# Performance work log

Hardware: AMD Instinct MI355X
Metric: run time of the kernel (lower is better)

Reference implementation:

```python
import jax, jax.numpy as jnp
import numpy as np

B, H, SQ, SK, D, INT, F = 1, 32, 2048, 2048, 128, 128, 32
THOLD = 0.5


def _mlp(x, W1, b1, W2, b2, W3, b3):
    # x: [b,h,s,d]; W*: [h,out,in] (torch Linear layout), y = x @ W^T + b, per head
    h = jax.nn.silu(jnp.einsum('bhsd,hid->bhsi', x, W1) + b1[None, :, None, :])
    h = jax.nn.silu(jnp.einsum('bhsi,hji->bhsj', h, W2) + b2[None, :, None, :])
    return jnp.einsum('bhsj,hfj->bhsf', h, W3) + b3[None, :, None, :]


def setup_inputs() -> dict:
    key = jax.random.key(0)
    ks = jax.random.split(key, 16)
    sc = 0.05  # small init so tanh stays in its linear-ish range
    inp = {
        'K': jax.random.normal(ks[0], (B, H, SK, D), jnp.float32),
        'Q': jax.random.normal(ks[1], (B, H, SQ, D), jnp.float32),
        'Wk1': jax.random.normal(ks[2], (H, INT, D), jnp.float32) * sc,
        'bk1': jax.random.normal(ks[3], (H, INT), jnp.float32) * sc,
        'Wk2': jax.random.normal(ks[4], (H, INT, INT), jnp.float32) * sc,
        'bk2': jax.random.normal(ks[5], (H, INT), jnp.float32) * sc,
        'Wk3': jax.random.normal(ks[6], (H, F, INT), jnp.float32) * sc,
        'bk3': jax.random.normal(ks[7], (H, F), jnp.float32) * sc,
        'Wq1': jax.random.normal(ks[8], (H, INT, D), jnp.float32) * sc,
        'bq1': jax.random.normal(ks[9], (H, INT), jnp.float32) * sc,
        'Wq2': jax.random.normal(ks[10], (H, INT, INT), jnp.float32) * sc,
        'bq2': jax.random.normal(ks[11], (H, INT), jnp.float32) * sc,
        'Wq3': jax.random.normal(ks[12], (H, F, INT), jnp.float32) * sc,
        'bq3': jax.random.normal(ks[13], (H, F), jnp.float32) * sc,
    }
    return inp


def reference(K, Q, Wk1, bk1, Wk2, bk2, Wk3, bk3, Wq1, bq1, Wq2, bq2, Wq3, bq3):
    # soft (hard=False) path of USA.forward
    Kl = jnp.tanh(_mlp(K, Wk1, bk1, Wk2, bk2, Wk3, bk3))  # [b,h,sk,F]
    Ql = jnp.tanh(_mlp(Q, Wq1, bq1, Wq2, bq2, Wq3, bq3))  # [b,h,sq,F]
    scores = jnp.einsum('bhtf,bhsf->bhts', Ql, Kl)        # [b,h,sq,sk]
    sq, sk = Q.shape[2], K.shape[2]
    causal = jnp.tril(jnp.ones((sq, sk), dtype=bool), k=sk - sq)
    mask_val = jnp.asarray(jnp.finfo(scores.dtype).min, scores.dtype)
    scores = jnp.where(causal[None, None], scores, mask_val)
    return jax.nn.sigmoid(scores - THOLD)
```

## Files before the change

### kernel.cpp

```cpp
#include <hip/hip_runtime.h>

#define NH  32
#define SEQ 2048
#define DIM 128
#define FD  32

typedef short          short8 __attribute__((ext_vector_type(8)));
typedef float          f32x4  __attribute__((ext_vector_type(4)));
typedef unsigned short u16x8  __attribute__((ext_vector_type(8)));

static __device__ __forceinline__ unsigned short f2bf(float f) {
    unsigned int u = __builtin_bit_cast(unsigned int, f);
    u += 0x7fffu + ((u >> 16) & 1u);
    return (unsigned short)(u >> 16);
}
static __device__ __forceinline__ float fexp(float x) {
    return __builtin_amdgcn_exp2f(x * 1.44269504088896f);
}
static __device__ __forceinline__ float sigm(float x) {
    return __builtin_amdgcn_rcpf(1.0f + fexp(-x));
}
static __device__ __forceinline__ float silu_f(float x) { return x * sigm(x); }
static __device__ __forceinline__ float tanh_f(float x) {
    return 1.0f - 2.0f * __builtin_amdgcn_rcpf(fexp(2.0f * x) + 1.0f);
}

#define WPH 36864
#define WPS (32 * WPH)

__global__ __launch_bounds__(256) void prep_weights(
    const float* __restrict__ Wk1, const float* __restrict__ Wk2,
    const float* __restrict__ Wk3, const float* __restrict__ Wq1,
    const float* __restrict__ Wq2, const float* __restrict__ Wq3,
    unsigned short* __restrict__ wimg) {
    int c = blockIdx.x * 256 + threadIdx.x;
    int s = (c >= 147456) ? 1 : 0;
    c -= s * 147456;
    const float* src;
    int dst;
    int sB = s * WPS;
    if (c < 65536) {
        int h = c >> 11, idx = c & 2047;
        int r = idx >> 4, jb = (idx & 15) * 8;
        src = (s ? Wq1 : Wk1) + h * 16384 + r * 128 + jb;
        dst = sB + h * WPH + r * 128 + (jb ^ ((r & 7) << 3));
    } else if (c < 131072) {
        int cc = c - 65536;
        int h = cc >> 11, idx = cc & 2047;
        int r = idx >> 4, jb = (idx & 15) * 8;
        src = (s ? Wq2 : Wk2) + h * 16384 + r * 128 + jb;
        dst = sB + h * WPH + 16384 + r * 128 + (jb ^ ((r & 7) << 3));
    } else {
        int cc = c - 131072;
        int h = cc >> 9, idx = cc & 511;
        int r = idx >> 4, jb = (idx & 15) * 8;
        src = (s ? Wq3 : Wk3) + h * 4096 + r * 128 + jb;
        dst = sB + h * WPH + 32768 + r * 128 + (jb ^ ((r & 7) << 3));
    }
    f32x4 u0 = *(const f32x4*)src;
    f32x4 u1 = *(const f32x4*)(src + 4);
    u16x8 p;
    p[0] = f2bf(u0[0]); p[1] = f2bf(u0[1]); p[2] = f2bf(u0[2]); p[3] = f2bf(u0[3]);
    p[4] = f2bf(u1[0]); p[5] = f2bf(u1[1]); p[6] = f2bf(u1[2]); p[7] = f2bf(u1[3]);
    *(u16x8*)(&wimg[dst]) = p;
}

template <int OT, int ACT>
static __device__ __forceinline__ void compute_layer(
    const short8 a[4], const unsigned short* W,
    const float* __restrict__ bias, unsigned short* dst, int lane, int wid) {
    int r0 = lane & 15, q = lane >> 4, kb = q * 8;
#pragma unroll
    for (int ot = 0; ot < OT; ++ot) {
        int wrow = ot * 16 + r0;
        int sw   = (wrow & 7) << 3;
        short8 b[4];
#pragma unroll
        for (int ks = 0; ks < 4; ++ks)
            b[ks] = *(const short8*)(&W[wrow * 128 + ((ks * 32 + kb) ^ sw)]);
        f32x4 acc = {0.f, 0.f, 0.f, 0.f};
#pragma unroll
        for (int ks = 0; ks < 4; ++ks)
            acc = __builtin_amdgcn_mfma_f32_16x16x32_bf16(a[ks], b[ks], acc, 0, 0, 0);
        float bv = bias[wrow];
#pragma unroll
        for (int r = 0; r < 4; ++r) {
            float y = acc[r] + bv;
            float v = (ACT == 0) ? silu_f(y) : tanh_f(y);
            int orow = wid * 16 + q * 4 + r;
            int ocol = ot * 16 + r0;
            dst[orow * 128 + (ocol ^ ((orow & 7) << 3))] = f2bf(v);
        }
    }
}

static __device__ __forceinline__ void compute_layer3_reg(
    const short8 a[4], const short8 w3f[2][4],
    const float* __restrict__ bias, unsigned short* dst, int lane, int wid) {
    int r0 = lane & 15, q = lane >> 4;
#pragma unroll
    for (int ot = 0; ot < 2; ++ot) {
        f32x4 acc = {0.f, 0.f, 0.f, 0.f};
#pragma unroll
        for (int ks = 0; ks < 4; ++ks)
            acc = __builtin_amdgcn_mfma_f32_16x16x32_bf16(a[ks], w3f[ot][ks], acc, 0, 0, 0);
        float bv = bias[ot * 16 + r0];
#pragma unroll
        for (int r = 0; r < 4; ++r) {
            float v = tanh_f(acc[r] + bv);
            dst[(wid * 16 + q * 4 + r) * FD + ot * 16 + r0] = f2bf(v);
        }
    }
}

__global__ __launch_bounds__(256) void mlp_kernel(
    const float* __restrict__ K,  const float* __restrict__ Q,
    const float* __restrict__ bk1, const float* __restrict__ bk2,
    const float* __restrict__ bk3, const float* __restrict__ bq1,
    const float* __restrict__ bq2, const float* __restrict__ bq3,
    const unsigned short* __restrict__ wimg,
    unsigned short* __restrict__ Kl, unsigned short* __restrict__ Ql) {
    __shared__ unsigned short wb[128 * 128];
    __shared__ unsigned short act[64 * 128];
    __shared__ unsigned short outb[64 * FD];
    int raw = blockIdx.x;
    int bid = (raw & 7) * 256 + (raw >> 3);
    int tb  = bid & 31;
    int h   = (bid >> 5) & 31;
    int s   = bid >> 10;

    const float* X  = s ? Q : K;
    const unsigned short* Wb = wimg + s * WPS + h * WPH;
    const float* B1 = (s ? bq1 : bk1) + h * 128;
    const float* B2 = (s ? bq2 : bk2) + h * 128;
    const float* B3 = (s ? bq3 : bk3) + h * FD;
    unsigned short* gout = (s ? Ql : Kl) + ((size_t)h * SEQ + (size_t)tb * 64) * FD;

    int tid = threadIdx.x, lane = tid & 63, wid = tid >> 6;
    int r0 = lane & 15, kb = (lane >> 4) * 8;

    short8 w3f[2][4];
    {
        const unsigned short* W3g = Wb + 32768;
        int sw = (r0 & 7) << 3;
#pragma unroll
        for (int ot = 0; ot < 2; ++ot)
#pragma unroll
            for (int ks = 0; ks < 4; ++ks)
                w3f[ot][ks] = *(const short8*)(&W3g[(ot * 16 + r0) * 128 + ((ks * 32 + kb) ^ sw)]);
    }

    const u16x8* wsrc = (const u16x8*)Wb;
#pragma unroll
    for (int i = 0; i < 8; ++i)
        *(u16x8*)(&wb[(i * 256 + tid) * 8]) = wsrc[i * 256 + tid];

    short8 a[4];
    const float* xs = X + ((size_t)h * SEQ + (size_t)tb * 64) * DIM;
    int row = wid * 16 + r0;
#pragma unroll
    for (int ks = 0; ks < 4; ++ks) {
        const float* p = xs + row * 128 + ks * 32 + kb;
        f32x4 u0 = *(const f32x4*)p;
        f32x4 u1 = *(const f32x4*)(p + 4);
        short8 t;
        t[0] = f2bf(u0[0]); t[1] = f2bf(u0[1]); t[2] = f2bf(u0[2]); t[3] = f2bf(u0[3]);
        t[4] = f2bf(u1[0]); t[5] = f2bf(u1[1]); t[6] = f2bf(u1[2]); t[7] = f2bf(u1[3]);
        a[ks] = t;
    }
    __syncthreads();
    compute_layer<8, 0>(a, wb, B1, act, lane, wid);
    __syncthreads();
#pragma unroll
    for (int i = 0; i < 8; ++i)
        *(u16x8*)(&wb[(i * 256 + tid) * 8]) = wsrc[2048 + i * 256 + tid];
    __syncthreads();
    {
        int sw = (row & 7) << 3;
#pragma unroll
        for (int ks = 0; ks < 4; ++ks)
            a[ks] = *(const short8*)(&act[row * 128 + ((ks * 32 + kb) ^ sw)]);
    }
    compute_layer<8, 0>(a, wb, B2, act, lane, wid);
    {
        int sw = (row & 7) << 3;
#pragma unroll
        for (int ks = 0; ks < 4; ++ks)
            a[ks] = *(const short8*)(&act[row * 128 + ((ks * 32 + kb) ^ sw)]);
    }
    compute_layer3_reg(a, w3f, B3, outb, lane, wid);
    __syncthreads();
    *(u16x8*)(gout + tid * 8) = *(const u16x8*)(&outb[tid * 8]);
}

__global__ __launch_bounds__(256) void score_kernel(
    const unsigned short* __restrict__ Ql, const unsigned short* __restrict__ Kl,
    float* __restrict__ out) {
    int raw = blockIdx.x;
    int bid = (raw & 7) * 512 + (raw >> 3);
    int h   = bid >> 7;
    int i   = (bid >> 2) & 31;
    int j   = bid & 3;
    int tq0 = i * 64, tk0 = j * 512;
    int tid = threadIdx.x;
    float* ob = out + (size_t)h * SEQ * SEQ;

    if (tk0 > tq0 + 63) {
        f32x4 z = {0.f, 0.f, 0.f, 0.f};
#pragma unroll
        for (int it = 0; it < 8; ++it) {
            int row = tq0 + it * 8 + (tid >> 5);
            float* dst = ob + (size_t)row * SEQ + tk0 + (tid & 31) * 4;
#pragma unroll
            for (int rep = 0; rep < 4; ++rep)
                *(f32x4*)(dst + rep * 128) = z;
        }
        return;
    }
    bool diag = (tk0 + 511 > tq0);
    int lane = tid & 63;
    int w    = tid >> 6;
    int r0   = lane & 15;
    int q    = lane >> 4;
    int kb   = q * 8;

    short8 aq[4], bk[8];
#pragma unroll
    for (int p = 0; p < 4; ++p)
        aq[p] = *(const short8*)(Ql + ((size_t)h * SEQ + tq0 + p * 16 + r0) * FD + kb);
#pragma unroll
    for (int ct = 0; ct < 8; ++ct)
        bk[ct] = *(const short8*)(Kl + ((size_t)h * SEQ + tk0 + w * 128 + ct * 16 + r0) * FD + kb);

#pragma unroll
    for (int p = 0; p < 4; ++p) {
#pragma unroll
        for (int ct = 0; ct < 8; ++ct) {
            f32x4 acc = {0.f, 0.f, 0.f, 0.f};
            acc = __builtin_amdgcn_mfma_f32_16x16x32_bf16(aq[p], bk[ct], acc, 0, 0, 0);
            int colw = w * 128 + ct * 16 + r0;
            float* colp = ob + (size_t)(tq0 + p * 16 + q * 4) * SEQ + tk0 + colw;
#pragma unroll
            for (int r = 0; r < 4; ++r) {
                float o = sigm(acc[r] - 0.5f);
                if (diag && (tk0 + colw) > (tq0 + p * 16 + q * 4 + r)) o = 0.0f;
                colp[(size_t)r * SEQ] = o;
            }
        }
    }
}

extern "C" void kernel_launch(void* const* d_in, const int* in_sizes, int n_in,
                              void* d_out, int out_size, void* d_ws, size_t ws_size,
                              hipStream_t stream) {
    const float* K   = (const float*)d_in[0];
    const float* Q   = (const float*)d_in[1];
    const float* Wk1 = (const float*)d_in[2];
    const float* bk1 = (const float*)d_in[3];
    const float* Wk2 = (const float*)d_in[4];
    const float* bk2 = (const float*)d_in[5];
    const float* Wk3 = (const float*)d_in[6];
    const float* bk3 = (const float*)d_in[7];
    const float* Wq1 = (const float*)d_in[8];
    const float* bq1 = (const float*)d_in[9];
    const float* Wq2 = (const float*)d_in[10];
    const float* bq2 = (const float*)d_in[11];
    const float* Wq3 = (const float*)d_in[12];
    const float* bq3 = (const float*)d_in[13];

    unsigned short* Kl   = (unsigned short*)d_ws;
    unsigned short* Ql   = Kl + (size_t)NH * SEQ * FD;
    unsigned short* wimg = Ql + (size_t)NH * SEQ * FD;

    prep_weights<<<dim3(1152), dim3(256), 0, stream>>>(
        Wk1, Wk2, Wk3, Wq1, Wq2, Wq3, wimg);

    mlp_kernel<<<dim3(2 * NH * (SEQ / 64)), dim3(256), 0, stream>>>(
        K, Q, bk1, bk2, bk3, bq1, bq2, bq3, wimg, Kl, Ql);

    score_kernel<<<dim3(NH * 32 * 4), dim3(256), 0, stream>>>(
        Ql, Kl, (float*)d_out);
}
```

Before: 153.2 us.

## Stage score tiles in LDS for coalesced full-row stores, skip masked MFMAs

Each score block now covers a full 64-row strip across all 2048 keys. It computes only the causal (non-masked) 16x16 tiles, stages the sigmoid results as bf16 in swizzled LDS, then writes complete rows to global memory with contiguous 32-byte stores per thread. The aim is to replace the scattered per-column 4-byte stores with coalesced row writes and to avoid MFMA and sigmoid work above the diagonal. In exchange, outputs are rounded to bf16 before being widened back to fp32, which costs precision. The kernel also uses 64KB of LDS per block and launches a quarter as many blocks, which lowers occupancy and parallelism.

```diff
diff --git a/kernel.cpp b/kernel.cpp
--- a/kernel.cpp
+++ b/kernel.cpp
@@ -13,6 +13,10 @@
     unsigned int u = __builtin_bit_cast(unsigned int, f);
     u += 0x7fffu + ((u >> 16) & 1u);
     return (unsigned short)(u >> 16);
+}
+static __device__ __forceinline__ float bf2f(unsigned short b) {
+    unsigned int u = (unsigned int)b << 16;
+    return __builtin_bit_cast(float, u);
 }
 static __device__ __forceinline__ float fexp(float x) {
     return __builtin_amdgcn_exp2f(x * 1.44269504088896f);
@@ -197,56 +201,84 @@
     const unsigned short* __restrict__ Ql, const unsigned short* __restrict__ Kl,
     float* __restrict__ out) {
     int raw = blockIdx.x;
-    int bid = (raw & 7) * 512 + (raw >> 3);
-    int h   = bid >> 7;
-    int i   = (bid >> 2) & 31;
-    int j   = bid & 3;
-    int tq0 = i * 64, tk0 = j * 512;
+    int bid = (raw & 7) * 128 + (raw >> 3);
+    int h   = bid >> 5;
+    int i   = bid & 31;
+    int tq0 = i * 64;
     int tid = threadIdx.x;
     float* ob = out + (size_t)h * SEQ * SEQ;
-
-    if (tk0 > tq0 + 63) {
-        f32x4 z = {0.f, 0.f, 0.f, 0.f};
-#pragma unroll
-        for (int it = 0; it < 8; ++it) {
-            int row = tq0 + it * 8 + (tid >> 5);
-            float* dst = ob + (size_t)row * SEQ + tk0 + (tid & 31) * 4;
-#pragma unroll
-            for (int rep = 0; rep < 4; ++rep)
-                *(f32x4*)(dst + rep * 128) = z;
-        }
-        return;
-    }
-    bool diag = (tk0 + 511 > tq0);
+    const unsigned short* Qb = Ql + (size_t)h * SEQ * FD;
+    const unsigned short* Kb = Kl + (size_t)h * SEQ * FD;
+
+    __shared__ unsigned short sb[16 * 2048];
     int lane = tid & 63;
     int w    = tid >> 6;
     int r0   = lane & 15;
     int q    = lane >> 4;
     int kb   = q * 8;
 
-    short8 aq[4], bk[8];
+    short8 aq[4];
 #pragma unroll
     for (int p = 0; p < 4; ++p)
-        aq[p] = *(const short8*)(Ql + ((size_t)h * SEQ + tq0 + p * 16 + r0) * FD + kb);
-#pragma unroll
-    for (int ct = 0; ct < 8; ++ct)
-        bk[ct] = *(const short8*)(Kl + ((size_t)h * SEQ + tk0 + w * 128 + ct * 16 + r0) * FD + kb);
+        aq[p] = *(const short8*)(Qb + (size_t)(tq0 + p * 16 + r0) * FD + kb);
 
 #pragma unroll
     for (int p = 0; p < 4; ++p) {
-#pragma unroll
-        for (int ct = 0; ct < 8; ++ct) {
+        int rmax = tq0 + p * 16 + 15;
+        int base = w * 512;
+        int nct  = 0;
+        if (base <= rmax) {
+            nct = ((rmax - base) >> 4) + 1;
+            if (nct > 32) nct = 32;
+        }
+        for (int ct = 0; ct < nct; ++ct) {
+            int col0 = base + ct * 16;
+            short8 bk = *(const short8*)(Kb + (size_t)(col0 + r0) * FD + kb);
             f32x4 acc = {0.f, 0.f, 0.f, 0.f};
-            acc = __builtin_amdgcn_mfma_f32_16x16x32_bf16(aq[p], bk[ct], acc, 0, 0, 0);
-            int colw = w * 128 + ct * 16 + r0;
-            float* colp = ob + (size_t)(tq0 + p * 16 + q * 4) * SEQ + tk0 + colw;
+            acc = __builtin_amdgcn_mfma_f32_16x16x32_bf16(aq[p], bk, acc, 0, 0, 0);
+            int colw = col0 + r0;
+            int sc   = colw ^ (q << 4);
 #pragma unroll
             for (int r = 0; r < 4; ++r) {
+                int rowg = tq0 + p * 16 + q * 4 + r;
                 float o = sigm(acc[r] - 0.5f);
-                if (diag && (tk0 + colw) > (tq0 + p * 16 + q * 4 + r)) o = 0.0f;
-                colp[(size_t)r * SEQ] = o;
+                if (colw > rowg) o = 0.0f;
+                sb[(q * 4 + r) * 2048 + sc] = f2bf(o);
             }
         }
+        asm volatile("s_waitcnt lgkmcnt(0)" ::: "memory");
+        __builtin_amdgcn_s_barrier();
+        int c0 = tid * 8;
+#pragma unroll
+        for (int rr = 0; rr < 16; ++rr) {
+            int rowg = tq0 + p * 16 + rr;
+            float* dst = ob + (size_t)rowg * SEQ + c0;
+            if (c0 + 7 <= rowg) {
+                int sw = ((rr >> 2) & 3) << 4;
+                u16x8 v = *(const u16x8*)(&sb[rr * 2048 + (c0 ^ sw)]);
+                f32x4 v0, v1;
+#pragma unroll
+                for (int e = 0; e < 4; ++e) { v0[e] = bf2f(v[e]); v1[e] = bf2f(v[e + 4]); }
+                *(f32x4*)dst       = v0;
+                *(f32x4*)(dst + 4) = v1;
+            } else if (c0 > rowg) {
+                f32x4 z = {0.f, 0.f, 0.f, 0.f};
+                *(f32x4*)dst       = z;
+                *(f32x4*)(dst + 4) = z;
+            } else {
+                int sw = ((rr >> 2) & 3) << 4;
+                u16x8 v = *(const u16x8*)(&sb[rr * 2048 + (c0 ^ sw)]);
+                f32x4 v0, v1;
+#pragma unroll
+                for (int e = 0; e < 4; ++e) {
+                    v0[e] = (c0 + e     <= rowg) ? bf2f(v[e])     : 0.0f;
+                    v1[e] = (c0 + e + 4 <= rowg) ? bf2f(v[e + 4]) : 0.0f;
+                }
+                *(f32x4*)dst       = v0;
+                *(f32x4*)(dst + 4) = v1;
+            }
+        }
+        __builtin_amdgcn_s_barrier();
     }
 }
 
@@ -278,6 +310,6 @@
     mlp_kernel<<<dim3(2 * NH * (SEQ / 64)), dim3(256), 0, stream>>>(
         K, Q, bk1, bk2, bk3, bq1, bq2, bq3, wimg, Kl, Ql);
 
-    score_kernel<<<dim3(NH * 32 * 4), dim3(256), 0, stream>>>(
+    score_kernel<<<dim3(NH * 32), dim3(256), 0, stream>>>(
         Ql, Kl, (float*)d_out);
 }
```

Measured after the change: 236.3 us. 1.54x slower.
